# Optimization experiments

Hardware: AMD Instinct MI355X
Metric: run time of the kernel (lower is better)

The kernel has to match this reference:

```python
import jax, jax.numpy as jnp
import numpy as np

N_NODES = 50000
N_EDGES = 800000
IN_DIM, HID, OUT_DIM = 128, 64, 64


def setup_inputs() -> dict:
    key = jax.random.key(0)
    ks = jax.random.split(key, 12)
    inp = {
        "x": jax.random.normal(ks[0], (N_NODES, IN_DIM), dtype=jnp.float32),
        "edge_index": jax.random.randint(ks[1], (2, N_EDGES), 0, N_NODES, dtype=jnp.int32),
    }
    dims = [(IN_DIM, HID), (HID, HID), (HID, HID), (HID, HID), (HID, OUT_DIM)]
    for i, (di, do) in enumerate(dims, start=1):
        scale = (2.0 / (di + do)) ** 0.5  # glorot-like
        inp[f"W{i}"] = jax.random.normal(ks[1 + i], (di, do), dtype=jnp.float32) * scale
        inp[f"b{i}"] = jnp.zeros((do,), dtype=jnp.float32)
    return inp


def _edge_norm(edge_index, n_nodes):
    # GCNConv(improved=True): add self-loops with weight 2.0, symmetric norm.
    src, dst = edge_index[0], edge_index[1]
    loop = jnp.arange(n_nodes, dtype=edge_index.dtype)
    src_f = jnp.concatenate([src, loop])
    dst_f = jnp.concatenate([dst, loop])
    w = jnp.concatenate([
        jnp.ones((src.shape[0],), jnp.float32),
        jnp.full((n_nodes,), 2.0, jnp.float32),
    ])
    deg = jax.ops.segment_sum(w, dst_f, num_segments=n_nodes)
    dinv = jnp.where(deg > 0, jax.lax.rsqrt(deg), 0.0)
    norm = dinv[src_f] * w * dinv[dst_f]  # [E+N]
    return src_f, dst_f, norm


def reference(x, edge_index, W1, b1, W2, b2, W3, b3, W4, b4, W5, b5):
    n = x.shape[0]
    src_f, dst_f, norm = _edge_norm(edge_index, n)

    def conv(h, W, b):
        h = h @ W                                  # [N, d_out]
        msg = h[src_f] * norm[:, None]             # gather + edge normalize
        return jax.ops.segment_sum(msg, dst_f, num_segments=n) + b

    h = jax.nn.relu(conv(x, W1, b1))
    h = jax.nn.relu(conv(h, W2, b2))
    h = jax.nn.relu(conv(h, W3, b3))
    h = jax.nn.relu(conv(h, W4, b4))
    return conv(h, W5, b5)
```

## Files before the change

### kernel.cpp

```cpp
#include <hip/hip_runtime.h>

#define NN 50000
#define NE 800000

__device__ __forceinline__ float bf2f(unsigned short u) {
    union { unsigned int i; float f; } v; v.i = ((unsigned int)u) << 16; return v.f;
}
__device__ __forceinline__ unsigned short f2bf(float f) {
    union { float f; unsigned int i; } v; v.f = f;
    unsigned int r = v.i + 0x7fffu + ((v.i >> 16) & 1u);
    return (unsigned short)(r >> 16);
}

__global__ void k_zero(float4* __restrict__ p, int n16) {
    int i = blockIdx.x * 256 + threadIdx.x;
    if (i < n16) p[i] = make_float4(0.f, 0.f, 0.f, 0.f);
}


__global__ void k_count(const int* __restrict__ dst, int* __restrict__ cnt, int E) {
    int e = blockIdx.x * 256 + threadIdx.x;
    if (e < E) atomicAdd(&cnt[dst[e]], 1);
}

__global__ void k_dinv(const int* __restrict__ cnt, float* __restrict__ dinv, int N) {
    int i = blockIdx.x * 256 + threadIdx.x;
    if (i < N) dinv[i] = rsqrtf(2.0f + (float)cnt[i]);
}

__global__ void k_scanA(const int* __restrict__ cnt, int* __restrict__ row_ptr,
                        int* __restrict__ bsum, int N) {
    __shared__ int buf[256];
    int i = blockIdx.x * 256 + threadIdx.x;
    int v = (i < N) ? cnt[i] : 0;
    buf[threadIdx.x] = v;
    __syncthreads();
    for (int off = 1; off < 256; off <<= 1) {
        int t = (threadIdx.x >= off) ? buf[threadIdx.x - off] : 0;
        __syncthreads();
        buf[threadIdx.x] += t;
        __syncthreads();
    }
    if (i < N) row_ptr[i] = buf[threadIdx.x] - v;
    if (threadIdx.x == 255) bsum[blockIdx.x] = buf[255];
}

__global__ void k_scanB(int* __restrict__ bsum, int nb) {
    __shared__ int buf[256];
    int v = (threadIdx.x < nb) ? bsum[threadIdx.x] : 0;
    buf[threadIdx.x] = v;
    __syncthreads();
    for (int off = 1; off < 256; off <<= 1) {
        int t = (threadIdx.x >= off) ? buf[threadIdx.x - off] : 0;
        __syncthreads();
        buf[threadIdx.x] += t;
        __syncthreads();
    }
    if (threadIdx.x < nb) bsum[threadIdx.x] = buf[threadIdx.x] - v;
}

__global__ void k_scanC(int* __restrict__ row_ptr, const int* __restrict__ bsum,
                        int N, int E) {
    int i = blockIdx.x * 256 + threadIdx.x;
    if (i < N) row_ptr[i] += bsum[blockIdx.x];
    if (i == 0) row_ptr[N] = E;
}

__global__ void k_fill(const int* __restrict__ src, const int* __restrict__ dst,
                       const float* __restrict__ dinv, const int* __restrict__ row_ptr,
                       int* __restrict__ cursor, int2* __restrict__ csr, int E) {
    int e = blockIdx.x * 256 + threadIdx.x;
    if (e >= E) return;
    int s = src[e], d = dst[e];
    int pos = row_ptr[d] + atomicAdd(&cursor[d], 1);
    float nm = dinv[s] * dinv[d];
    csr[pos] = make_int2(s, __float_as_int(nm));
}


__global__ __launch_bounds__(256, 4) void k_gemm128(const float* __restrict__ X,
                                                    const float* __restrict__ W,
                                                    unsigned short* __restrict__ H, int N) {
    const int K = 128;
    __shared__ float Ws[K * 64];
    for (int i = threadIdx.x; i < K * 16; i += 256)
        ((float4*)Ws)[i] = ((const float4*)W)[i];
    __syncthreads();

    const int g  = threadIdx.x >> 3;
    const int c0 = (threadIdx.x & 7) * 8;
    const int r0 = blockIdx.x * 64 + g * 2;
    const int r1 = r0 + 1;
    const bool v0 = r0 < N, v1 = r1 < N;

    float a00=0,a01=0,a02=0,a03=0,a04=0,a05=0,a06=0,a07=0;
    float a10=0,a11=0,a12=0,a13=0,a14=0,a15=0,a16=0,a17=0;

    const float* x0 = X + (size_t)r0 * K;
    const float* x1 = X + (size_t)r1 * K;

#pragma unroll 1
    for (int k0 = 0; k0 < K; k0 += 4) {
        float4 xa = v0 ? *(const float4*)(x0 + k0) : make_float4(0, 0, 0, 0);
        float4 xb = v1 ? *(const float4*)(x1 + k0) : make_float4(0, 0, 0, 0);
#pragma unroll
        for (int kk = 0; kk < 4; ++kk) {
            const float xs0 = (kk == 0) ? xa.x : (kk == 1) ? xa.y : (kk == 2) ? xa.z : xa.w;
            const float xs1 = (kk == 0) ? xb.x : (kk == 1) ? xb.y : (kk == 2) ? xb.z : xb.w;
            const float* wr = &Ws[(k0 + kk) * 64 + c0];
            const float4 w0 = *(const float4*)(wr);
            const float4 w1 = *(const float4*)(wr + 4);
            a00 = fmaf(xs0, w0.x, a00); a01 = fmaf(xs0, w0.y, a01);
            a02 = fmaf(xs0, w0.z, a02); a03 = fmaf(xs0, w0.w, a03);
            a04 = fmaf(xs0, w1.x, a04); a05 = fmaf(xs0, w1.y, a05);
            a06 = fmaf(xs0, w1.z, a06); a07 = fmaf(xs0, w1.w, a07);
            a10 = fmaf(xs1, w0.x, a10); a11 = fmaf(xs1, w0.y, a11);
            a12 = fmaf(xs1, w0.z, a12); a13 = fmaf(xs1, w0.w, a13);
            a14 = fmaf(xs1, w1.x, a14); a15 = fmaf(xs1, w1.y, a15);
            a16 = fmaf(xs1, w1.z, a16); a17 = fmaf(xs1, w1.w, a17);
        }
    }

    if (v0) {
        uint4 p;
        p.x = (unsigned)f2bf(a00) | ((unsigned)f2bf(a01) << 16);
        p.y = (unsigned)f2bf(a02) | ((unsigned)f2bf(a03) << 16);
        p.z = (unsigned)f2bf(a04) | ((unsigned)f2bf(a05) << 16);
        p.w = (unsigned)f2bf(a06) | ((unsigned)f2bf(a07) << 16);
        *(uint4*)&H[(size_t)r0 * 64 + c0] = p;
    }
    if (v1) {
        uint4 p;
        p.x = (unsigned)f2bf(a10) | ((unsigned)f2bf(a11) << 16);
        p.y = (unsigned)f2bf(a12) | ((unsigned)f2bf(a13) << 16);
        p.z = (unsigned)f2bf(a14) | ((unsigned)f2bf(a15) << 16);
        p.w = (unsigned)f2bf(a16) | ((unsigned)f2bf(a17) << 16);
        *(uint4*)&H[(size_t)r1 * 64 + c0] = p;
    }
}


template <bool RELU>
__device__ __forceinline__ void agg_row2(const unsigned short* __restrict__ H,
                                         const long long* __restrict__ csr_ll,
                                         const float4& b4, float di0, float di1,
                                         int i0, int i1, int s0, int e0, int s1, int e1,
                                         int lane, int g, int c4,
                                         float4& r0, float4& r1) {
    ushort4 hs0 = *(const ushort4*)&H[(size_t)i0 * 64 + c4];
    ushort4 hs1 = *(const ushort4*)&H[(size_t)i1 * 64 + c4];

    int ee0 = s0 + lane, ee1 = s1 + lane;
    long long pk0 = (ee0 < e0) ? csr_ll[ee0] : 0LL;
    long long pk1 = (ee1 < e1) ? csr_ll[ee1] : 0LL;
    int px0 = (int)pk0, py0 = (int)(pk0 >> 32);
    int px1 = (int)pk1, py1 = (int)(pk1 >> 32);

    int m0 = e0 - s0; if (m0 > 64) m0 = 64;
    int m1 = e1 - s1; if (m1 > 64) m1 = 64;
    int nt0 = (m0 + 3) >> 2, nt1 = (m1 + 3) >> 2;
    int ntm = nt0 > nt1 ? nt0 : nt1;

    float4 acc0 = make_float4(0.f, 0.f, 0.f, 0.f);
    float4 acc1 = make_float4(0.f, 0.f, 0.f, 0.f);

#pragma unroll 4
    for (int t = 0; t < ntm; ++t) {
        int sl = t * 4 + g;
        if (t < nt0) {
            int ss   = __shfl(px0, sl);
            float nn = __uint_as_float(__shfl(py0, sl));
            ushort4 h = *(const ushort4*)&H[(size_t)ss * 64 + c4];
            acc0.x = fmaf(bf2f(h.x), nn, acc0.x);
            acc0.y = fmaf(bf2f(h.y), nn, acc0.y);
            acc0.z = fmaf(bf2f(h.z), nn, acc0.z);
            acc0.w = fmaf(bf2f(h.w), nn, acc0.w);
        }
        if (t < nt1) {
            int ss   = __shfl(px1, sl);
            float nn = __uint_as_float(__shfl(py1, sl));
            ushort4 h = *(const ushort4*)&H[(size_t)ss * 64 + c4];
            acc1.x = fmaf(bf2f(h.x), nn, acc1.x);
            acc1.y = fmaf(bf2f(h.y), nn, acc1.y);
            acc1.z = fmaf(bf2f(h.z), nn, acc1.z);
            acc1.w = fmaf(bf2f(h.w), nn, acc1.w);
        }
    }

    for (int base = s0 + 64; base < e0; base += 64) {
        int e = base + lane;
        long long pk = (e < e0) ? csr_ll[e] : 0LL;
        int px = (int)pk, py = (int)(pk >> 32);
        int m = e0 - base; if (m > 64) m = 64;
        int nt = (m + 3) >> 2;
        for (int t = 0; t < nt; ++t) {
            int sl = t * 4 + g;
            int ss = __shfl(px, sl);
            float nn = __uint_as_float(__shfl(py, sl));
            ushort4 h = *(const ushort4*)&H[(size_t)ss * 64 + c4];
            acc0.x = fmaf(bf2f(h.x), nn, acc0.x);
            acc0.y = fmaf(bf2f(h.y), nn, acc0.y);
            acc0.z = fmaf(bf2f(h.z), nn, acc0.z);
            acc0.w = fmaf(bf2f(h.w), nn, acc0.w);
        }
    }
    for (int base = s1 + 64; base < e1; base += 64) {
        int e = base + lane;
        long long pk = (e < e1) ? csr_ll[e] : 0LL;
        int px = (int)pk, py = (int)(pk >> 32);
        int m = e1 - base; if (m > 64) m = 64;
        int nt = (m + 3) >> 2;
        for (int t = 0; t < nt; ++t) {
            int sl = t * 4 + g;
            int ss = __shfl(px, sl);
            float nn = __uint_as_float(__shfl(py, sl));
            ushort4 h = *(const ushort4*)&H[(size_t)ss * 64 + c4];
            acc1.x = fmaf(bf2f(h.x), nn, acc1.x);
            acc1.y = fmaf(bf2f(h.y), nn, acc1.y);
            acc1.z = fmaf(bf2f(h.z), nn, acc1.z);
            acc1.w = fmaf(bf2f(h.w), nn, acc1.w);
        }
    }

#pragma unroll
    for (int d = 16; d <= 32; d <<= 1) {
        acc0.x += __shfl_xor(acc0.x, d); acc0.y += __shfl_xor(acc0.y, d);
        acc0.z += __shfl_xor(acc0.z, d); acc0.w += __shfl_xor(acc0.w, d);
        acc1.x += __shfl_xor(acc1.x, d); acc1.y += __shfl_xor(acc1.y, d);
        acc1.z += __shfl_xor(acc1.z, d); acc1.w += __shfl_xor(acc1.w, d);
    }

    float sa = 2.0f * di0 * di0, sb = 2.0f * di1 * di1;
    r0.x = acc0.x + sa * bf2f(hs0.x) + b4.x;
    r0.y = acc0.y + sa * bf2f(hs0.y) + b4.y;
    r0.z = acc0.z + sa * bf2f(hs0.z) + b4.z;
    r0.w = acc0.w + sa * bf2f(hs0.w) + b4.w;
    r1.x = acc1.x + sb * bf2f(hs1.x) + b4.x;
    r1.y = acc1.y + sb * bf2f(hs1.y) + b4.y;
    r1.z = acc1.z + sb * bf2f(hs1.z) + b4.z;
    r1.w = acc1.w + sb * bf2f(hs1.w) + b4.w;
    if (RELU) {
        r0.x = fmaxf(r0.x, 0.f); r0.y = fmaxf(r0.y, 0.f);
        r0.z = fmaxf(r0.z, 0.f); r0.w = fmaxf(r0.w, 0.f);
        r1.x = fmaxf(r1.x, 0.f); r1.y = fmaxf(r1.y, 0.f);
        r1.z = fmaxf(r1.z, 0.f); r1.w = fmaxf(r1.w, 0.f);
    }
}

__global__ __launch_bounds__(256, 6) void k_fused(const unsigned short* __restrict__ H,
                                                  const int* __restrict__ row_ptr,
                                                  const long long* __restrict__ csr_ll,
                                                  const float* __restrict__ dinv,
                                                  const float* __restrict__ bias,
                                                  const float* __restrict__ Wn,
                                                  unsigned short* __restrict__ Hout, int N) {
    __shared__ float Wl[64 * 64];
    __shared__ float Al[4][2][64];

    const int wid  = threadIdx.x >> 6;
    const int lane = threadIdx.x & 63;
    const int i0   = (blockIdx.x * 4 + wid) * 2;
    const int i1   = i0 + 1;
    const int g    = lane >> 4;
    const int c4   = (lane & 15) * 4;

    int idx = i0 + lane;
    int   rp = (lane <= 2) ? row_ptr[idx] : 0;
    float dv = (lane <  2) ? dinv[idx]    : 0.f;

    for (int t = threadIdx.x; t < 1024; t += 256)
        ((float4*)Wl)[t] = ((const float4*)Wn)[t];

    const float4 b4 = *(const float4*)&bias[c4];
    int s0 = __shfl(rp, 0), sm = __shfl(rp, 1), e1 = __shfl(rp, 2);
    float di0 = __shfl(dv, 0), di1 = __shfl(dv, 1);

    float4 r0, r1;
    agg_row2<true>(H, csr_ll, b4, di0, di1, i0, i1, s0, sm, sm, e1,
                   lane, g, c4, r0, r1);

    __syncthreads();
    if (g == 0) {
        *(float4*)&Al[wid][0][c4] = r0;
        *(float4*)&Al[wid][1][c4] = r1;
    }
    __syncthreads();

    float y0 = 0.f, y1 = 0.f;
#pragma unroll 4
    for (int c = 0; c < 64; c += 4) {
        float4 a0 = *(const float4*)&Al[wid][0][c];
        float4 a1 = *(const float4*)&Al[wid][1][c];
        float w0 = Wl[(c + 0) * 64 + lane];
        float w1 = Wl[(c + 1) * 64 + lane];
        float w2 = Wl[(c + 2) * 64 + lane];
        float w3 = Wl[(c + 3) * 64 + lane];
        y0 = fmaf(a0.x, w0, y0); y0 = fmaf(a0.y, w1, y0);
        y0 = fmaf(a0.z, w2, y0); y0 = fmaf(a0.w, w3, y0);
        y1 = fmaf(a1.x, w0, y1); y1 = fmaf(a1.y, w1, y1);
        y1 = fmaf(a1.z, w2, y1); y1 = fmaf(a1.w, w3, y1);
    }
    Hout[(size_t)i0 * 64 + lane] = f2bf(y0);
    Hout[(size_t)i1 * 64 + lane] = f2bf(y1);
}

__global__ __launch_bounds__(256, 8) void k_agg_last(const unsigned short* __restrict__ H,
                                                     const int* __restrict__ row_ptr,
                                                     const long long* __restrict__ csr_ll,
                                                     const float* __restrict__ dinv,
                                                     const float* __restrict__ bias,
                                                     float* __restrict__ out, int N) {
    const int wid  = threadIdx.x >> 6;
    const int lane = threadIdx.x & 63;
    const int i0   = (blockIdx.x * 4 + wid) * 2;
    const int i1   = i0 + 1;
    const int g    = lane >> 4;
    const int c4   = (lane & 15) * 4;

    const float4 b4 = *(const float4*)&bias[c4];

    int idx = i0 + lane;
    int   rp = (lane <= 2) ? row_ptr[idx] : 0;
    float dv = (lane <  2) ? dinv[idx]    : 0.f;
    int s0 = __shfl(rp, 0), sm = __shfl(rp, 1), e1 = __shfl(rp, 2);
    float di0 = __shfl(dv, 0), di1 = __shfl(dv, 1);

    float4 r0, r1;
    agg_row2<false>(H, csr_ll, b4, di0, di1, i0, i1, s0, sm, sm, e1,
                    lane, g, c4, r0, r1);
    if (g == 0) {
        *(float4*)&out[(size_t)i0 * 64 + c4] = r0;
        *(float4*)&out[(size_t)i1 * 64 + c4] = r1;
    }
}


extern "C" void kernel_launch(void* const* d_in, const int* in_sizes, int n_in,
                              void* d_out, int out_size, void* d_ws, size_t ws_size,
                              hipStream_t stream) {
    (void)in_sizes; (void)n_in; (void)out_size; (void)ws_size;

    const float* x  = (const float*)d_in[0];
    const int*   ei = (const int*)d_in[1];
    const float* Wl[5] = {(const float*)d_in[2], (const float*)d_in[4], (const float*)d_in[6],
                          (const float*)d_in[8], (const float*)d_in[10]};
    const float* bl[5] = {(const float*)d_in[3], (const float*)d_in[5], (const float*)d_in[7],
                          (const float*)d_in[9], (const float*)d_in[11]};
    float* out = (float*)d_out;

    const int* src = ei;
    const int* dst = ei + NE;

    char* ws = (char*)d_ws;
    size_t off = 0;
    auto alloc = [&](size_t bytes) -> void* {
        void* p = ws + off;
        off += (bytes + 255) & ~(size_t)255;
        return p;
    };
    int*   cnt      = (int*)alloc(NN * 4);
    int*   cursor   = (int*)alloc(NN * 4);
    size_t zero_bytes = (size_t)((char*)(cursor + NN) - (char*)cnt);
    int*   row_ptr  = (int*)alloc((NN + 1) * 4);
    int*   bsum     = (int*)alloc(256 * 4);
    float* dinv     = (float*)alloc(NN * 4);
    int2*  csr      = (int2*)alloc((size_t)NE * 8);
    unsigned short* Hb  = (unsigned short*)alloc((size_t)NN * 64 * 2);
    unsigned short* Hb2 = (unsigned short*)alloc((size_t)NN * 64 * 2);

    int n16 = (int)((zero_bytes + 15) / 16);
    k_zero<<<(n16 + 255) / 256, 256, 0, stream>>>((float4*)cnt, n16);

    int ebl = (NE + 255) / 256;
    int nbl = (NN + 255) / 256;
    k_count<<<ebl, 256, 0, stream>>>(dst, cnt, NE);
    k_dinv<<<nbl, 256, 0, stream>>>(cnt, dinv, NN);
    k_scanA<<<nbl, 256, 0, stream>>>(cnt, row_ptr, bsum, NN);
    k_scanB<<<1, 256, 0, stream>>>(bsum, nbl);
    k_scanC<<<nbl, 256, 0, stream>>>(row_ptr, bsum, NN, NE);
    k_fill<<<ebl, 256, 0, stream>>>(src, dst, dinv, row_ptr, cursor, csr, NE);

    const long long* csr_ll = (const long long*)csr;
    int gg = (NN + 63) / 64;
    int ga = NN / 8;

    k_gemm128<<<gg, 256, 0, stream>>>(x, Wl[0], Hb, NN);
    k_fused<<<ga, 256, 0, stream>>>(Hb,  row_ptr, csr_ll, dinv, bl[0], Wl[1], Hb2, NN);
    k_fused<<<ga, 256, 0, stream>>>(Hb2, row_ptr, csr_ll, dinv, bl[1], Wl[2], Hb,  NN);
    k_fused<<<ga, 256, 0, stream>>>(Hb,  row_ptr, csr_ll, dinv, bl[2], Wl[3], Hb2, NN);
    k_fused<<<ga, 256, 0, stream>>>(Hb2, row_ptr, csr_ll, dinv, bl[3], Wl[4], Hb,  NN);
    k_agg_last<<<ga, 256, 0, stream>>>(Hb, row_ptr, csr_ll, dinv, bl[4], out, NN);
}
```

Before: 296.0 us.

## Replace LDS staging in fused GEMV with readlane broadcasts and direct weight loads

The fused aggregate+transform kernel no longer stages the 16KB weight matrix and the aggregated rows in shared memory. Each lane broadcasts its aggregated values with v_readlane and reads weights straight from global memory, which should hit in cache. This removes two block barriers and the LDS footprint, and the launch bound rises to 8 waves per SIMD. In exchange there are 64 global weight loads per lane and 128 scalar readlanes instead of LDS reads, and any latency from those cached loads is exposed.

```diff
diff --git a/kernel.cpp b/kernel.cpp
--- a/kernel.cpp
+++ b/kernel.cpp
@@ -10,6 +10,9 @@
     union { float f; unsigned int i; } v; v.f = f;
     unsigned int r = v.i + 0x7fffu + ((v.i >> 16) & 1u);
     return (unsigned short)(r >> 16);
+}
+__device__ __forceinline__ float rdlane_f(float x, int l) {
+    return __uint_as_float(__builtin_amdgcn_readlane(__float_as_uint(x), l));
 }
 
 __global__ void k_zero(float4* __restrict__ p, int n16) {
@@ -247,16 +250,13 @@
     }
 }
 
-__global__ __launch_bounds__(256, 6) void k_fused(const unsigned short* __restrict__ H,
+__global__ __launch_bounds__(256, 8) void k_fused(const unsigned short* __restrict__ H,
                                                   const int* __restrict__ row_ptr,
                                                   const long long* __restrict__ csr_ll,
                                                   const float* __restrict__ dinv,
                                                   const float* __restrict__ bias,
                                                   const float* __restrict__ Wn,
                                                   unsigned short* __restrict__ Hout, int N) {
-    __shared__ float Wl[64 * 64];
-    __shared__ float Al[4][2][64];
-
     const int wid  = threadIdx.x >> 6;
     const int lane = threadIdx.x & 63;
     const int i0   = (blockIdx.x * 4 + wid) * 2;
@@ -268,9 +268,6 @@
     int   rp = (lane <= 2) ? row_ptr[idx] : 0;
     float dv = (lane <  2) ? dinv[idx]    : 0.f;
 
-    for (int t = threadIdx.x; t < 1024; t += 256)
-        ((float4*)Wl)[t] = ((const float4*)Wn)[t];
-
     const float4 b4 = *(const float4*)&bias[c4];
     int s0 = __shfl(rp, 0), sm = __shfl(rp, 1), e1 = __shfl(rp, 2);
     float di0 = __shfl(dv, 0), di1 = __shfl(dv, 1);
@@ -279,26 +276,21 @@
     agg_row2<true>(H, csr_ll, b4, di0, di1, i0, i1, s0, sm, sm, e1,
                    lane, g, c4, r0, r1);
 
-    __syncthreads();
-    if (g == 0) {
-        *(float4*)&Al[wid][0][c4] = r0;
-        *(float4*)&Al[wid][1][c4] = r1;
-    }
-    __syncthreads();
-
     float y0 = 0.f, y1 = 0.f;
-#pragma unroll 4
-    for (int c = 0; c < 64; c += 4) {
-        float4 a0 = *(const float4*)&Al[wid][0][c];
-        float4 a1 = *(const float4*)&Al[wid][1][c];
-        float w0 = Wl[(c + 0) * 64 + lane];
-        float w1 = Wl[(c + 1) * 64 + lane];
-        float w2 = Wl[(c + 2) * 64 + lane];
-        float w3 = Wl[(c + 3) * 64 + lane];
-        y0 = fmaf(a0.x, w0, y0); y0 = fmaf(a0.y, w1, y0);
-        y0 = fmaf(a0.z, w2, y0); y0 = fmaf(a0.w, w3, y0);
-        y1 = fmaf(a1.x, w0, y1); y1 = fmaf(a1.y, w1, y1);
-        y1 = fmaf(a1.z, w2, y1); y1 = fmaf(a1.w, w3, y1);
+#pragma unroll
+    for (int q = 0; q < 16; ++q) {
+        float w0 = Wn[(4 * q + 0) * 64 + lane];
+        float w1 = Wn[(4 * q + 1) * 64 + lane];
+        float w2 = Wn[(4 * q + 2) * 64 + lane];
+        float w3 = Wn[(4 * q + 3) * 64 + lane];
+        y0 = fmaf(rdlane_f(r0.x, q), w0, y0);
+        y0 = fmaf(rdlane_f(r0.y, q), w1, y0);
+        y0 = fmaf(rdlane_f(r0.z, q), w2, y0);
+        y0 = fmaf(rdlane_f(r0.w, q), w3, y0);
+        y1 = fmaf(rdlane_f(r1.x, q), w0, y1);
+        y1 = fmaf(rdlane_f(r1.y, q), w1, y1);
+        y1 = fmaf(rdlane_f(r1.z, q), w2, y1);
+        y1 = fmaf(rdlane_f(r1.w, q), w3, y1);
     }
     Hout[(size_t)i0 * 64 + lane] = f2bf(y0);
     Hout[(size_t)i1 * 64 + lane] = f2bf(y1);
```

Measured after the change: 273.8 us. 7.5% less time.
